# Kernel optimization log

Measured on AMD Instinct MI355X. Metric: run time of the kernel, lower is better.

Reference implementation:

```python
import jax, jax.numpy as jnp
import numpy as np

NUM_HEADS = 8
D_CONV = 4
NORMALIZER = 16.0
LN_EPS = 1e-5


def setup_inputs() -> dict:
    key = jax.random.key(0)
    ks = jax.random.split(key, 9)
    B, L, E = 4, 2048, 1024
    dk = E // 2
    return {
        "x": jax.random.normal(ks[0], (B, L, E), jnp.float32),
        "conv_w": jax.random.normal(ks[1], (E, D_CONV), jnp.float32) * 0.3,
        "wq": jax.random.normal(ks[2], (E, dk), jnp.float32) * 0.02,
        "wkg": jax.random.normal(ks[3], (E, dk), jnp.float32) * 0.02,
        "wv": jax.random.normal(ks[4], (E, E), jnp.float32) * 0.02,
        "wg": jax.random.normal(ks[5], (E, E), jnp.float32) * 0.02,
        "bg": jax.random.normal(ks[6], (E,), jnp.float32) * 0.02,
        "wout": jax.random.normal(ks[7], (E, E), jnp.float32) * 0.02,
        "aug_balance": jax.random.normal(ks[8], (dk,), jnp.float32) * 0.1,
    }


def _causal_dwconv_silu(x, w):
    # x: [B, L, E]; w: [E, W] depthwise kernel. Causal: left-pad W-1 zeros.
    xt = jnp.transpose(x, (0, 2, 1))  # [B, E, L]
    y = jax.lax.conv_general_dilated(
        xt, w[:, None, :], window_strides=(1,), padding=[(w.shape[1] - 1, 0)],
        feature_group_count=x.shape[-1], dimension_numbers=("NCH", "OIH", "NCH"))
    return jnp.transpose(jax.nn.silu(y), (0, 2, 1))  # [B, L, E]


def _gla(q, k, v, gk, scale):
    # Gated linear attention recurrence (fused_chunk_gla math):
    #   S_t = S_{t-1} * exp(gk_t)[:, None] + k_t (outer) v_t
    #   o_t = (scale * q_t) @ S_t
    # q, k, gk: [B,H,L,Dk]; v: [B,H,L,Dv]
    B, H, L, Dk = q.shape
    Dv = v.shape[-1]

    def step(S, inp):
        qt, kt, vt, gt = inp  # [B,H,Dk], [B,H,Dk], [B,H,Dv], [B,H,Dk]
        S = S * jnp.exp(gt)[..., None] + kt[..., None] * vt[..., None, :]
        ot = jnp.einsum("bhk,bhkv->bhv", qt * scale, S)
        return S, ot

    mv = lambda a: jnp.moveaxis(a, 2, 0)  # L to leading axis for scan
    S0 = jnp.zeros((B, H, Dk, Dv), q.dtype)
    _, o = jax.lax.scan(step, S0, (mv(q), mv(k), mv(v), mv(gk)))
    return jnp.moveaxis(o, 0, 2)  # [B,H,L,Dv]


def reference(x, conv_w, wq, wkg, wv, wg, bg, wout, aug_balance):
    B, L, E = x.shape
    H = NUM_HEADS
    xc = _causal_dwconv_silu(x, conv_w)
    q = xc @ wq            # [B,L,dk]
    kg = xc @ wkg          # [B,L,dk]
    v = xc @ wv            # [B,L,E]
    g = xc @ wg + bg       # [B,L,E]

    gk = jax.nn.log_sigmoid(kg) / NORMALIZER
    k = 1.0 - jnp.exp(gk)

    dkh = q.shape[-1] // H  # key_dim per head
    to_heads = lambda t: t.reshape(B, L, H, -1).transpose(0, 2, 1, 3)
    qh, kh, vh, gkh = to_heads(q), to_heads(k), to_heads(v), to_heads(gk)

    scale = dkh ** -0.5
    o = _gla(qh, kh, vh, gkh, scale)  # [B,H,L,head_dim]

    # Augmented term: aug_w[b,h,l] = sum_d q[b,h,l,d] * aug[h,d] * k[b,h,l,d]
    aug = aug_balance.reshape(H, dkh)
    aug_w = jnp.einsum("bhld,hd,bhld->bhl", qh, aug, kh)
    o = o + jax.nn.sigmoid(aug_w[..., None] * vh)

    # LayerNorm over head_dim, no affine
    mu = o.mean(-1, keepdims=True)
    var = o.var(-1, keepdims=True)
    o = (o - mu) * jax.lax.rsqrt(var + LN_EPS)

    o = o.transpose(0, 2, 1, 3).reshape(B, L, E)
    return (jax.nn.silu(g) * o) @ wout
```

## Files before the change

kernel.cpp:

```cpp
#include <hip/hip_runtime.h>
#include <stdint.h>

typedef unsigned short u16;
typedef unsigned int u32;
typedef __attribute__((ext_vector_type(4))) float f32x4;
typedef __attribute__((ext_vector_type(8))) short short8;
typedef __attribute__((ext_vector_type(8))) _Float16 f16x8;

#define H 8
#define LSEQ 2048
#define E 1024
#define DK 512
#define DVH 128
#define DKH 64
#define NCHUNK 32
#define MROWS 8192
#define LN_EPS 1e-5f

static __device__ __forceinline__ float bf2f(u16 u) {
    union { float f; u32 i; } v; v.i = ((u32)u) << 16; return v.f;
}
static __device__ __forceinline__ u16 f2bf(float f) {
    union { float f; u32 i; } v; v.f = f;
    u32 r = v.i + 0x7FFFu + ((v.i >> 16) & 1u);
    return (u16)(r >> 16);
}

__global__ __launch_bounds__(256) void k_conv(const float* __restrict__ x,
                                              const float* __restrict__ cw,
                                              u16* __restrict__ xc) {
    const int l0 = blockIdx.x * 64;
    const int c  = blockIdx.y * 256 + threadIdx.x;
    const int b  = blockIdx.z;
    const f32x4 w = *(const f32x4*)(cw + c * 4);
    const float* base = x + (size_t)b * LSEQ * E + c;
    u16* ob = xc + (size_t)b * LSEQ * E + c;
    float x3 = (l0 >= 3) ? base[(size_t)(l0 - 3) * E] : 0.f;
    float x2 = (l0 >= 2) ? base[(size_t)(l0 - 2) * E] : 0.f;
    float x1 = (l0 >= 1) ? base[(size_t)(l0 - 1) * E] : 0.f;
#pragma unroll 8
    for (int r = 0; r < 64; r++) {
        const float x0 = base[(size_t)(l0 + r) * E];
        float a = x3 * w[0];
        a = fmaf(x2, w[1], a);
        a = fmaf(x1, w[2], a);
        a = fmaf(x0, w[3], a);
        const float s = a / (1.f + __expf(-a));
        ob[(size_t)(l0 + r) * E] = f2bf(s);
        x3 = x2; x2 = x1; x1 = x0;
    }
}

__global__ __launch_bounds__(256) void k_transpose_all(const float* __restrict__ wq,
                                                       const float* __restrict__ wkg,
                                                       const float* __restrict__ wv,
                                                       const float* __restrict__ wg,
                                                       const float* __restrict__ wout,
                                                       u16* __restrict__ wcat,
                                                       u16* __restrict__ woutT) {
    __shared__ float tile[32][33];
    const int z = blockIdx.z;
    const float* src; u16* dst; int Ncols;
    if (z == 0)      { src = wq;   dst = wcat;                        Ncols = 512; }
    else if (z == 1) { src = wkg;  dst = wcat + (size_t)512 * 1024;   Ncols = 512; }
    else if (z == 2) { src = wv;   dst = wcat + (size_t)1024 * 1024;  Ncols = 1024; }
    else if (z == 3) { src = wg;   dst = wcat + (size_t)2048 * 1024;  Ncols = 1024; }
    else             { src = wout; dst = woutT;                       Ncols = 1024; }
    const int n0 = blockIdx.x * 32, k0 = blockIdx.y * 32;
    if (n0 >= Ncols) return;
    const int K = 1024;
    const int tx = threadIdx.x & 31, ty = threadIdx.x >> 5;
#pragma unroll
    for (int p = 0; p < 4; p++) {
        const int r = p * 8 + ty;
        tile[r][tx] = src[(size_t)(k0 + r) * Ncols + n0 + tx];
    }
    __syncthreads();
#pragma unroll
    for (int p = 0; p < 4; p++) {
        const int rn = p * 8 + ty;
        dst[(size_t)(n0 + rn) * K + k0 + tx] = f2bf(tile[tx][rn]);
    }
}

__global__ __launch_bounds__(512, 1) void k_gemm0(const u16* __restrict__ A,
                                                  const u16* __restrict__ Bt,
                                                  u16* __restrict__ oQ, u16* __restrict__ oKG,
                                                  u16* __restrict__ oV, u16* __restrict__ oSG,
                                                  const float* __restrict__ bg) {
    const int K = 1024;
    __shared__ __align__(16) u16 smem[4][16384];
    const int tid = threadIdx.x;
    const int lane = tid & 63, wv = tid >> 6;
    const int wm = wv >> 2, wn = wv & 3;

    const int id = blockIdx.x;
    const int local = id >> 3;
    const int bx = ((id & 7) << 3) | (local & 7);
    const int by = local >> 3;

    const size_t rowBase = (size_t)bx * 128;
    const size_t colBase = (size_t)by * 384;

    const int rowIn = lane >> 2;
    const int uIn = lane & 3;

    auto stageA = [&](int hh) {
        u16* slotA = &smem[hh & 3][0];
        const u16* g = A + rowBase * K + hh * 32;
        const int row = wv * 16 + rowIn;
        const int sg = uIn ^ ((row >> 1) & 3);
        __builtin_amdgcn_global_load_lds(
            (const __attribute__((address_space(1))) void*)(g + (size_t)row * K + sg * 8),
            (__attribute__((address_space(3))) void*)(slotA + wv * 512), 16, 0, 0);
    };
    auto stageB = [&](int hh) {
        u16* slotB = &smem[hh & 3][4096];
        const u16* g = Bt + colBase * K + hh * 32;
#pragma unroll
        for (int i = 0; i < 3; i++) {
            const int row = i * 128 + wv * 16 + rowIn;
            const int sg = uIn ^ ((row >> 1) & 3);
            __builtin_amdgcn_global_load_lds(
                (const __attribute__((address_space(1))) void*)(g + (size_t)row * K + sg * 8),
                (__attribute__((address_space(3))) void*)(slotB + i * 4096 + wv * 512), 16, 0, 0);
        }
    };

    f32x4 acc[4][6];
#pragma unroll
    for (int m = 0; m < 4; m++)
#pragma unroll
        for (int n = 0; n < 6; n++) acc[m][n] = (f32x4){0.f, 0.f, 0.f, 0.f};

    const int rsub = lane & 15;
    const int cgl = lane >> 4;

    stageA(0); stageB(0);
    stageA(1); stageB(1);
    stageA(2); stageB(2);

    const int NT2 = K >> 5;
    for (int h = 0; h < NT2; h++) {
        const int rem = NT2 - 1 - h;
        if (rem >= 2)      asm volatile("s_waitcnt vmcnt(8)" ::: "memory");
        else if (rem == 1) asm volatile("s_waitcnt vmcnt(4)" ::: "memory");
        else               asm volatile("s_waitcnt vmcnt(0)" ::: "memory");
        asm volatile("s_barrier" ::: "memory");
        const u16* As = &smem[h & 3][0];
        const u16* Bs = As + 4096;
        short8 af[4], bfr[6];
#pragma unroll
        for (int mi = 0; mi < 4; mi++) {
            const int row = wm * 64 + mi * 16 + rsub;
            const int g = cgl ^ ((row >> 1) & 3);
            af[mi] = *(const short8*)(As + row * 32 + g * 8);
        }
#pragma unroll
        for (int ni = 0; ni < 6; ni++) {
            const int row = wn * 96 + ni * 16 + rsub;
            const int g = cgl ^ ((row >> 1) & 3);
            bfr[ni] = *(const short8*)(Bs + row * 32 + g * 8);
        }
        if (h + 3 < NT2) { stageA(h + 3); stageB(h + 3); }
        __builtin_amdgcn_s_setprio(1);
#pragma unroll
        for (int mi = 0; mi < 4; mi++)
#pragma unroll
            for (int ni = 0; ni < 6; ni++)
                acc[mi][ni] = __builtin_amdgcn_mfma_f32_16x16x32_bf16(af[mi], bfr[ni], acc[mi][ni], 0, 0, 0);
        __builtin_amdgcn_s_setprio(0);
    }

    const int r0 = (lane >> 4) * 4;
    u16* lds = &smem[0][0];
    __syncthreads();
#pragma unroll
    for (int ni = 0; ni < 6; ni++) {
        const int colg = (int)colBase + wn * 96 + ni * 16 + rsub;
        const bool isSG = (colg >= 2048);
        const float bgv = isSG ? bg[colg - 2048] : 0.f;
#pragma unroll
        for (int mi = 0; mi < 4; mi++) {
            const int lcol = wn * 96 + ni * 16 + rsub;
#pragma unroll
            for (int r = 0; r < 4; r++) {
                const int lrow = wm * 64 + mi * 16 + r0 + r;
                float val = acc[mi][ni][r];
                if (isSG) { const float y = val + bgv; val = y / (1.f + __expf(-y)); }
                lds[lrow * 384 + lcol] = f2bf(val);
            }
        }
    }
    __syncthreads();
    if (lane < 48) {
        const int col = (int)colBase + lane * 8;
        u16* seg; int stride; int c0;
        if (col < 512)       { seg = oQ;  stride = 512;  c0 = col; }
        else if (col < 1024) { seg = oKG; stride = 512;  c0 = col - 512; }
        else if (col < 2048) { seg = oV;  stride = 1024; c0 = col - 1024; }
        else                 { seg = oSG; stride = 1024; c0 = col - 2048; }
#pragma unroll
        for (int rr = 0; rr < 16; rr++) {
            const int lrow = wv * 16 + rr;
            const uint4 vv = *(const uint4*)(lds + lrow * 384 + lane * 8);
            *(uint4*)(seg + (rowBase + lrow) * (size_t)stride + c0) = vv;
        }
    }
}

__global__ __launch_bounds__(512, 1) void k_gemm1(const u16* __restrict__ A,
                                                  const u16* __restrict__ Bt,
                                                  float* __restrict__ oF) {
    const int K = 1024, N = 1024;
    __shared__ __align__(16) u16 smem[4][12288];
    const int tid = threadIdx.x;
    const int lane = tid & 63, wv = tid >> 6;
    const int wm = wv >> 1, wn = wv & 1;

    const int id = blockIdx.y * gridDim.x + blockIdx.x;
    const int bx = ((id & 7) << 2) | ((id >> 3) & 3);
    const int by = id >> 5;

    const size_t rowBase = (size_t)bx * 256;
    const size_t colBase = (size_t)by * 128;

    auto stageA = [&](int hh) {
        u16* slotA = &smem[hh & 3][0];
        const u16* g = A + rowBase * K + hh * 32;
#pragma unroll
        for (int i = 0; i < 2; i++) {
            const int r = i * 128 + wv * 16 + (lane >> 2);
            const int sg = (lane & 3) ^ ((r >> 1) & 3);
            __builtin_amdgcn_global_load_lds(
                (const __attribute__((address_space(1))) void*)(g + (size_t)r * K + sg * 8),
                (__attribute__((address_space(3))) void*)(slotA + i * 4096 + wv * 512), 16, 0, 0);
        }
    };
    auto stageB = [&](int hh) {
        u16* slotB = &smem[hh & 3][8192];
        const u16* g = Bt + colBase * K + hh * 32;
        const int r = wv * 16 + (lane >> 2);
        const int sg = (lane & 3) ^ ((r >> 1) & 3);
        __builtin_amdgcn_global_load_lds(
            (const __attribute__((address_space(1))) void*)(g + (size_t)r * K + sg * 8),
            (__attribute__((address_space(3))) void*)(slotB + wv * 512), 16, 0, 0);
    };

    f32x4 acc[4][4];
#pragma unroll
    for (int m = 0; m < 4; m++)
#pragma unroll
        for (int n = 0; n < 4; n++) acc[m][n] = (f32x4){0.f, 0.f, 0.f, 0.f};

    const int rsub = lane & 15;
    const int cgl = lane >> 4;

    stageA(0); stageB(0);
    stageA(1); stageB(1);
    stageA(2); stageB(2);

    const int NT2 = K >> 5;
    for (int h = 0; h < NT2; h++) {
        const int rem = NT2 - 1 - h;
        if (rem >= 2)      asm volatile("s_waitcnt vmcnt(6)" ::: "memory");
        else if (rem == 1) asm volatile("s_waitcnt vmcnt(3)" ::: "memory");
        else               asm volatile("s_waitcnt vmcnt(0)" ::: "memory");
        asm volatile("s_barrier" ::: "memory");
        const u16* As = &smem[h & 3][0];
        const u16* Bs = As + 8192;
        short8 af[4], bfr[4];
#pragma unroll
        for (int mi = 0; mi < 4; mi++) {
            const int row = wm * 64 + mi * 16 + rsub;
            const int g = cgl ^ ((row >> 1) & 3);
            af[mi] = *(const short8*)(As + row * 32 + g * 8);
        }
#pragma unroll
        for (int ni = 0; ni < 4; ni++) {
            const int row = wn * 64 + ni * 16 + rsub;
            const int g = cgl ^ ((row >> 1) & 3);
            bfr[ni] = *(const short8*)(Bs + row * 32 + g * 8);
        }
        if (h + 3 < NT2) { stageA(h + 3); stageB(h + 3); }
        __builtin_amdgcn_s_setprio(1);
#pragma unroll
        for (int mi = 0; mi < 4; mi++)
#pragma unroll
            for (int ni = 0; ni < 4; ni++)
                acc[mi][ni] = __builtin_amdgcn_mfma_f32_16x16x32_bf16(af[mi], bfr[ni], acc[mi][ni], 0, 0, 0);
        __builtin_amdgcn_s_setprio(0);
    }

    const int r0 = (lane >> 4) * 4;
#pragma unroll
    for (int mi = 0; mi < 4; mi++)
#pragma unroll
        for (int ni = 0; ni < 4; ni++) {
            const size_t col = colBase + wn * 64 + ni * 16 + rsub;
#pragma unroll
            for (int r = 0; r < 4; r++) {
                const size_t row = rowBase + wm * 64 + mi * 16 + r0 + r;
                oF[row * (size_t)N + col] = acc[mi][ni][r];
            }
        }
}

__global__ __launch_bounds__(256) void k_gla1(const u16* __restrict__ q,
                                              const u16* __restrict__ kg,
                                              const u16* __restrict__ v,
                                              const float* __restrict__ aug,
                                              u16* __restrict__ qt,
                                              u16* __restrict__ obuf,
                                              float* __restrict__ Sd,
                                              float* __restrict__ Dc,
                                              float* __restrict__ augw) {
    __shared__ __align__(16) float    s_f[64][68];
    __shared__ __align__(16) _Float16 s_q[64][72];
    __shared__ __align__(16) _Float16 s_k[64][72];
    __shared__ __align__(16) _Float16 s_kT[64][72];
    __shared__ __align__(16) _Float16 s_a[64][72];
    __shared__ __align__(16) _Float16 s_vT[128][72];
    const int c = blockIdx.x, bh = blockIdx.y;
    const int b = bh >> 3, h = bh & 7;
    const int tid = threadIdx.x;
    const size_t rowBase = (size_t)b * LSEQ + c * 64;
    const size_t sdBase = (size_t)bh * NCHUNK + c;

    const int tA = tid >> 2, g4 = tid & 3;
    uint4 qr0, qr1;
    {
        const int d0 = g4 * 16;
        const u16* kp = kg + (rowBase + tA) * DK + h * 64 + d0;
        const uint4 k0 = *(const uint4*)kp;
        const uint4 k1 = *(const uint4*)(kp + 8);
        const u16 kv[16] = {
            (u16)(k0.x & 0xffff), (u16)(k0.x >> 16), (u16)(k0.y & 0xffff), (u16)(k0.y >> 16),
            (u16)(k0.z & 0xffff), (u16)(k0.z >> 16), (u16)(k0.w & 0xffff), (u16)(k0.w >> 16),
            (u16)(k1.x & 0xffff), (u16)(k1.x >> 16), (u16)(k1.y & 0xffff), (u16)(k1.y >> 16),
            (u16)(k1.z & 0xffff), (u16)(k1.z >> 16), (u16)(k1.w & 0xffff), (u16)(k1.w >> 16) };
#pragma unroll
        for (int j = 0; j < 16; j++) {
            const float xk = bf2f(kv[j]);
            const float ls = fminf(xk, 0.f) - __logf(1.f + __expf(-fabsf(xk)));
            s_f[tA][d0 + j] = ls * (1.f / 16.f);
        }
        const u16* qp = q + (rowBase + tA) * DK + h * 64 + d0;
        qr0 = *(const uint4*)qp;
        qr1 = *(const uint4*)(qp + 8);

        const int dv0 = g4 * 32;
        const u16* vp = v + (rowBase + tA) * E + h * 128 + dv0;
#pragma unroll
        for (int j8 = 0; j8 < 32; j8 += 8) {
            const uint4 u = *(const uint4*)(vp + j8);
            s_vT[dv0 + j8 + 0][tA] = (_Float16)bf2f((u16)(u.x & 0xffff));
            s_vT[dv0 + j8 + 1][tA] = (_Float16)bf2f((u16)(u.x >> 16));
            s_vT[dv0 + j8 + 2][tA] = (_Float16)bf2f((u16)(u.y & 0xffff));
            s_vT[dv0 + j8 + 3][tA] = (_Float16)bf2f((u16)(u.y >> 16));
            s_vT[dv0 + j8 + 4][tA] = (_Float16)bf2f((u16)(u.z & 0xffff));
            s_vT[dv0 + j8 + 5][tA] = (_Float16)bf2f((u16)(u.z >> 16));
            s_vT[dv0 + j8 + 6][tA] = (_Float16)bf2f((u16)(u.w & 0xffff));
            s_vT[dv0 + j8 + 7][tA] = (_Float16)bf2f((u16)(u.w >> 16));
        }
    }
    __syncthreads();

    {
        const int d = tid >> 2, qseg = tid & 3;
        float part = 0.f;
#pragma unroll
        for (int j = 0; j < 16; j++) part += s_f[qseg * 16 + j][d];
        float incl = part;
        const float u1 = __shfl_up(incl, 1, 4); if (qseg >= 1) incl += u1;
        const float u2 = __shfl_up(incl, 2, 4); if (qseg >= 2) incl += u2;
        float run = incl - part;
#pragma unroll
        for (int j = 0; j < 16; j++) {
            const int t = qseg * 16 + j;
            const float g = s_f[t][d];
            run += g;
            const float kk = 1.f - __expf(g);
            const float ktil = kk * __expf(-run);
            s_k[t][d] = (_Float16)ktil;
            s_kT[d][t] = (_Float16)ktil;
            s_a[t][d] = (_Float16)kk;
            s_f[t][d] = run;
        }
    }
    __syncthreads();

    {
        const int t = tA, d0 = g4 * 16;
        const u16 qv16[16] = {
            (u16)(qr0.x & 0xffff), (u16)(qr0.x >> 16), (u16)(qr0.y & 0xffff), (u16)(qr0.y >> 16),
            (u16)(qr0.z & 0xffff), (u16)(qr0.z >> 16), (u16)(qr0.w & 0xffff), (u16)(qr0.w >> 16),
            (u16)(qr1.x & 0xffff), (u16)(qr1.x >> 16), (u16)(qr1.y & 0xffff), (u16)(qr1.y >> 16),
            (u16)(qr1.z & 0xffff), (u16)(qr1.z >> 16), (u16)(qr1.w & 0xffff), (u16)(qr1.w >> 16) };
        float qv[16];
        float augp = 0.f;
#pragma unroll
        for (int j = 0; j < 16; j++) {
            const int d = d0 + j;
            const float qraw = bf2f(qv16[j]);
            const float L = s_f[t][d];
            const float kk = (float)s_a[t][d];
            const float qtv = qraw * __expf(L) * 0.125f;
            s_q[t][d] = (_Float16)qtv;
            qv[j] = qtv;
            augp = fmaf(qraw * aug[h * 64 + d], kk, augp);
        }
        u16* qto = qt + (rowBase + t) * DK + h * 64 + d0;
#pragma unroll
        for (int j8 = 0; j8 < 16; j8 += 8) {
            uint4 u;
            u.x = (u32)f2bf(qv[j8 + 0]) | ((u32)f2bf(qv[j8 + 1]) << 16);
            u.y = (u32)f2bf(qv[j8 + 2]) | ((u32)f2bf(qv[j8 + 3]) << 16);
            u.z = (u32)f2bf(qv[j8 + 4]) | ((u32)f2bf(qv[j8 + 5]) << 16);
            u.w = (u32)f2bf(qv[j8 + 6]) | ((u32)f2bf(qv[j8 + 7]) << 16);
            *(uint4*)(qto + j8) = u;
        }
        augp += __shfl_xor(augp, 1);
        augp += __shfl_xor(augp, 2);
        if ((tid & 3) == 0) augw[(size_t)bh * LSEQ + c * 64 + t] = augp;
    }
    __syncthreads();

    const int wv = tid >> 6, lane = tid & 63;
    const int rsub = lane & 15, kq8 = (lane >> 4) * 8, r0 = (lane >> 4) * 4;
    {
#pragma unroll
        for (int si = 0; si < 4; si++) {
            if (si <= wv) {
                f32x4 acc = (f32x4){0.f, 0.f, 0.f, 0.f};
#pragma unroll
                for (int kk = 0; kk < 2; kk++) {
                    const f16x8 af = *(const f16x8*)&s_q[wv * 16 + rsub][kk * 32 + kq8];
                    const f16x8 bf = *(const f16x8*)&s_k[si * 16 + rsub][kk * 32 + kq8];
                    acc = __builtin_amdgcn_mfma_f32_16x16x32_f16(af, bf, acc, 0, 0, 0);
                }
                const int scol = si * 16 + rsub;
#pragma unroll
                for (int r = 0; r < 4; r++) {
                    const int trow = wv * 16 + r0 + r;
                    const float val = (scol <= trow) ? acc[r] : 0.f;
                    s_a[trow][scol] = (_Float16)val;
                }
            } else {
#pragma unroll
                for (int r = 0; r < 4; r++)
                    s_a[wv * 16 + r0 + r][si * 16 + rsub] = (_Float16)0.f;
            }
        }
    }
    __syncthreads();

    {
        f32x4 oacc[8];
#pragma unroll
        for (int n = 0; n < 8; n++) oacc[n] = (f32x4){0.f, 0.f, 0.f, 0.f};
        const f16x8 a0 = *(const f16x8*)&s_a[wv * 16 + rsub][kq8];
        const f16x8 a1 = *(const f16x8*)&s_a[wv * 16 + rsub][32 + kq8];
#pragma unroll
        for (int n = 0; n < 8; n++) {
            const f16x8 b0 = *(const f16x8*)&s_vT[n * 16 + rsub][kq8];
            const f16x8 b1 = *(const f16x8*)&s_vT[n * 16 + rsub][32 + kq8];
            oacc[n] = __builtin_amdgcn_mfma_f32_16x16x32_f16(a0, b0, oacc[n], 0, 0, 0);
            oacc[n] = __builtin_amdgcn_mfma_f32_16x16x32_f16(a1, b1, oacc[n], 0, 0, 0);
        }
        u16* ob = obuf + ((size_t)bh * LSEQ + c * 64) * DVH;
#pragma unroll
        for (int n = 0; n < 8; n++) {
            const int dv = n * 16 + rsub;
#pragma unroll
            for (int r = 0; r < 4; r++) {
                const int trow = wv * 16 + r0 + r;
                ob[(size_t)trow * DVH + dv] = f2bf(oacc[n][r]);
            }
        }
    }

    {
        f32x4 sacc[8];
#pragma unroll
        for (int n = 0; n < 8; n++) sacc[n] = (f32x4){0.f, 0.f, 0.f, 0.f};
        const f16x8 a0 = *(const f16x8*)&s_kT[wv * 16 + rsub][kq8];
        const f16x8 a1 = *(const f16x8*)&s_kT[wv * 16 + rsub][32 + kq8];
#pragma unroll
        for (int n = 0; n < 8; n++) {
            const f16x8 b0 = *(const f16x8*)&s_vT[n * 16 + rsub][kq8];
            const f16x8 b1 = *(const f16x8*)&s_vT[n * 16 + rsub][32 + kq8];
            sacc[n] = __builtin_amdgcn_mfma_f32_16x16x32_f16(a0, b0, sacc[n], 0, 0, 0);
            sacc[n] = __builtin_amdgcn_mfma_f32_16x16x32_f16(a1, b1, sacc[n], 0, 0, 0);
        }
        float dend[4];
#pragma unroll
        for (int r = 0; r < 4; r++) dend[r] = __expf(s_f[63][wv * 16 + r0 + r]);
#pragma unroll
        for (int n = 0; n < 8; n++) {
            const int dv = n * 16 + rsub;
#pragma unroll
            for (int r = 0; r < 4; r++) {
                const int d = wv * 16 + r0 + r;
                Sd[(sdBase * DKH + d) * DVH + dv] = sacc[n][r] * dend[r];
            }
        }
        if (rsub == 0) {
#pragma unroll
            for (int r = 0; r < 4; r++) {
                const int d = wv * 16 + r0 + r;
                Dc[sdBase * DKH + d] = dend[r];
            }
        }
    }
}

__global__ __launch_bounds__(256) void k_gla2(const float* __restrict__ Sd,
                                              u16* __restrict__ Ss,
                                              const float* __restrict__ Dc) {
    const int cid = blockIdx.x * 256 + threadIdx.x;
    const int bh = cid >> 13;
    const int e = cid & 8191;
    const int d = e >> 7;
    float run = 0.f;
    const size_t base = (size_t)bh * NCHUNK * 8192 + e;
    for (int c = 0; c < NCHUNK; c++) {
        const size_t idx = base + (size_t)c * 8192;
        const float dl = Sd[idx];
        Ss[idx] = f2bf(run);
        run = fmaf(Dc[((size_t)bh * NCHUNK + c) * DKH + d], run, dl);
    }
}

__global__ __launch_bounds__(256) void k_gla3(const u16* __restrict__ qt,
                                              const u16* __restrict__ v,
                                              const u16* __restrict__ sg,
                                              const u16* __restrict__ obuf,
                                              const u16* __restrict__ Ss,
                                              const float* __restrict__ augw,
                                              u16* __restrict__ a2) {
    __shared__ __align__(16) _Float16 s_ST[128][72];
    __shared__ __align__(16) _Float16 s_qr[64][72];
    __shared__ __align__(16) float    s_O2[64][132];
    const int c = blockIdx.x, bh = blockIdx.y;
    const int b = bh >> 3, h = bh & 7;
    const int tid = threadIdx.x;
    const size_t rowBase = (size_t)b * LSEQ + c * 64;
    {
        const int d = tid >> 2, dv0 = (tid & 3) * 32;
        const u16* sp = Ss + (((size_t)bh * NCHUNK + c) * DKH + d) * DVH + dv0;
#pragma unroll
        for (int j8 = 0; j8 < 32; j8 += 8) {
            const uint4 u = *(const uint4*)(sp + j8);
            s_ST[dv0 + j8 + 0][d] = (_Float16)bf2f((u16)(u.x & 0xffff));
            s_ST[dv0 + j8 + 1][d] = (_Float16)bf2f((u16)(u.x >> 16));
            s_ST[dv0 + j8 + 2][d] = (_Float16)bf2f((u16)(u.y & 0xffff));
            s_ST[dv0 + j8 + 3][d] = (_Float16)bf2f((u16)(u.y >> 16));
            s_ST[dv0 + j8 + 4][d] = (_Float16)bf2f((u16)(u.z & 0xffff));
            s_ST[dv0 + j8 + 5][d] = (_Float16)bf2f((u16)(u.z >> 16));
            s_ST[dv0 + j8 + 6][d] = (_Float16)bf2f((u16)(u.w & 0xffff));
            s_ST[dv0 + j8 + 7][d] = (_Float16)bf2f((u16)(u.w >> 16));
        }
    }
    {
        const int t = tid >> 2, d0 = (tid & 3) * 16;
        const u16* qp = qt + (rowBase + t) * DK + h * 64 + d0;
        const uint4 q0 = *(const uint4*)qp;
        const uint4 q1 = *(const uint4*)(qp + 8);
        const u16 qv[16] = {
            (u16)(q0.x & 0xffff), (u16)(q0.x >> 16), (u16)(q0.y & 0xffff), (u16)(q0.y >> 16),
            (u16)(q0.z & 0xffff), (u16)(q0.z >> 16), (u16)(q0.w & 0xffff), (u16)(q0.w >> 16),
            (u16)(q1.x & 0xffff), (u16)(q1.x >> 16), (u16)(q1.y & 0xffff), (u16)(q1.y >> 16),
            (u16)(q1.z & 0xffff), (u16)(q1.z >> 16), (u16)(q1.w & 0xffff), (u16)(q1.w >> 16) };
#pragma unroll
        for (int j = 0; j < 16; j++) s_qr[t][d0 + j] = (_Float16)bf2f(qv[j]);
    }
    __syncthreads();
    {
        const int wv = tid >> 6, lane = tid & 63;
        const int rsub = lane & 15, kq8 = (lane >> 4) * 8, r0 = (lane >> 4) * 4;
        const f16x8 a0 = *(const f16x8*)&s_qr[wv * 16 + rsub][kq8];
        const f16x8 a1 = *(const f16x8*)&s_qr[wv * 16 + rsub][32 + kq8];
#pragma unroll
        for (int n = 0; n < 8; n++) {
            f32x4 acc = (f32x4){0.f, 0.f, 0.f, 0.f};
            const f16x8 b0 = *(const f16x8*)&s_ST[n * 16 + rsub][kq8];
            const f16x8 b1 = *(const f16x8*)&s_ST[n * 16 + rsub][32 + kq8];
            acc = __builtin_amdgcn_mfma_f32_16x16x32_f16(a0, b0, acc, 0, 0, 0);
            acc = __builtin_amdgcn_mfma_f32_16x16x32_f16(a1, b1, acc, 0, 0, 0);
            const int dv = n * 16 + rsub;
#pragma unroll
            for (int r = 0; r < 4; r++) s_O2[wv * 16 + r0 + r][dv] = acc[r];
        }
    }
    __syncthreads();
    const int t = tid >> 2, dv0 = (tid & 3) * 32;
    float o[32];
    const u16* op = obuf + ((size_t)bh * LSEQ + c * 64 + t) * DVH + dv0;
#pragma unroll
    for (int j8 = 0; j8 < 32; j8 += 8) {
        const uint4 u = *(const uint4*)(op + j8);
        o[j8 + 0] = bf2f((u16)(u.x & 0xffff)); o[j8 + 1] = bf2f((u16)(u.x >> 16));
        o[j8 + 2] = bf2f((u16)(u.y & 0xffff)); o[j8 + 3] = bf2f((u16)(u.y >> 16));
        o[j8 + 4] = bf2f((u16)(u.z & 0xffff)); o[j8 + 5] = bf2f((u16)(u.z >> 16));
        o[j8 + 6] = bf2f((u16)(u.w & 0xffff)); o[j8 + 7] = bf2f((u16)(u.w >> 16));
    }
#pragma unroll
    for (int j = 0; j < 32; j += 4) {
        const f32x4 sv = *(const f32x4*)&s_O2[t][dv0 + j];
        o[j + 0] += sv[0]; o[j + 1] += sv[1]; o[j + 2] += sv[2]; o[j + 3] += sv[3];
    }
    const float aw = augw[(size_t)bh * LSEQ + c * 64 + t];
    const u16* vp = v + (rowBase + t) * E + h * 128 + dv0;
#pragma unroll
    for (int j8 = 0; j8 < 32; j8 += 8) {
        const uint4 u = *(const uint4*)(vp + j8);
        const float vv[8] = {
            bf2f((u16)(u.x & 0xffff)), bf2f((u16)(u.x >> 16)),
            bf2f((u16)(u.y & 0xffff)), bf2f((u16)(u.y >> 16)),
            bf2f((u16)(u.z & 0xffff)), bf2f((u16)(u.z >> 16)),
            bf2f((u16)(u.w & 0xffff)), bf2f((u16)(u.w >> 16)) };
#pragma unroll
        for (int j = 0; j < 8; j++)
            o[j8 + j] += 1.f / (1.f + __expf(-aw * vv[j]));
    }
    float sum = 0.f;
#pragma unroll
    for (int j = 0; j < 32; j++) sum += o[j];
    sum += __shfl_xor(sum, 1); sum += __shfl_xor(sum, 2);
    const float mu = sum * (1.f / 128.f);
    float sq = 0.f;
#pragma unroll
    for (int j = 0; j < 32; j++) { const float dlt = o[j] - mu; sq = fmaf(dlt, dlt, sq); }
    sq += __shfl_xor(sq, 1); sq += __shfl_xor(sq, 2);
    const float rs = rsqrtf(sq * (1.f / 128.f) + LN_EPS);
    const u16* sp2 = sg + (rowBase + t) * E + h * 128 + dv0;
    u16* ap = a2 + (rowBase + t) * E + h * 128 + dv0;
#pragma unroll
    for (int j8 = 0; j8 < 32; j8 += 8) {
        const uint4 us = *(const uint4*)(sp2 + j8);
        const float sv[8] = {
            bf2f((u16)(us.x & 0xffff)), bf2f((u16)(us.x >> 16)),
            bf2f((u16)(us.y & 0xffff)), bf2f((u16)(us.y >> 16)),
            bf2f((u16)(us.z & 0xffff)), bf2f((u16)(us.z >> 16)),
            bf2f((u16)(us.w & 0xffff)), bf2f((u16)(us.w >> 16)) };
        uint4 u;
        u.x = (u32)f2bf(sv[0] * ((o[j8 + 0] - mu) * rs)) | ((u32)f2bf(sv[1] * ((o[j8 + 1] - mu) * rs)) << 16);
        u.y = (u32)f2bf(sv[2] * ((o[j8 + 2] - mu) * rs)) | ((u32)f2bf(sv[3] * ((o[j8 + 3] - mu) * rs)) << 16);
        u.z = (u32)f2bf(sv[4] * ((o[j8 + 4] - mu) * rs)) | ((u32)f2bf(sv[5] * ((o[j8 + 5] - mu) * rs)) << 16);
        u.w = (u32)f2bf(sv[6] * ((o[j8 + 6] - mu) * rs)) | ((u32)f2bf(sv[7] * ((o[j8 + 7] - mu) * rs)) << 16);
        *(uint4*)(ap + j8) = u;
    }
}

extern "C" void kernel_launch(void* const* d_in, const int* in_sizes, int n_in,
                              void* d_out, int out_size, void* d_ws, size_t ws_size,
                              hipStream_t stream) {
    const float* x      = (const float*)d_in[0];
    const float* conv_w = (const float*)d_in[1];
    const float* wq     = (const float*)d_in[2];
    const float* wkg    = (const float*)d_in[3];
    const float* wv     = (const float*)d_in[4];
    const float* wg     = (const float*)d_in[5];
    const float* bg     = (const float*)d_in[6];
    const float* wout   = (const float*)d_in[7];
    const float* aug    = (const float*)d_in[8];

    char* ws = (char*)d_ws;
    size_t off = 0;
    auto alloc = [&](size_t bytes) -> char* {
        char* p = ws + off;
        off += (bytes + 255) & ~(size_t)255;
        return p;
    };
    u16* xc    = (u16*)alloc((size_t)MROWS * E * 2);
    u16* wcat  = (u16*)alloc((size_t)3072 * E * 2);
    u16* woutT = (u16*)alloc((size_t)E * E * 2);
    u16* qb    = (u16*)alloc((size_t)MROWS * DK * 2);
    u16* kgb   = (u16*)alloc((size_t)MROWS * DK * 2);
    u16* vb    = (u16*)alloc((size_t)MROWS * E * 2);
    u16* sgb   = (u16*)alloc((size_t)MROWS * E * 2);
    u16* qtb   = (u16*)alloc((size_t)MROWS * DK * 2);
    u16* obuf  = (u16*)alloc((size_t)32 * LSEQ * DVH * 2);
    u16* Ssb   = (u16*)alloc((size_t)32 * NCHUNK * DKH * DVH * 2);
    float* Dc  = (float*)alloc((size_t)32 * NCHUNK * DKH * 4);
    float* augw= (float*)alloc((size_t)32 * LSEQ * 4);
    u16* a2    = qb;
    float* Sd  = (float*)d_out;

    k_conv<<<dim3(LSEQ / 64, E / 256, 4), 256, 0, stream>>>(x, conv_w, xc);
    k_transpose_all<<<dim3(32, 32, 5), 256, 0, stream>>>(wq, wkg, wv, wg, wout, wcat, woutT);
    k_gemm0<<<512, 512, 0, stream>>>(xc, wcat, qb, kgb, vb, sgb, bg);
    k_gla1<<<dim3(NCHUNK, 32), 256, 0, stream>>>(qb, kgb, vb, aug, qtb, obuf, Sd, Dc, augw);
    k_gla2<<<1024, 256, 0, stream>>>(Sd, Ssb, Dc);
    k_gla3<<<dim3(NCHUNK, 32), 256, 0, stream>>>(qtb, vb, sgb, obuf, Ssb, augw, a2);
    k_gemm1<<<dim3(32, 8), 512, 0, stream>>>(a2, woutT, (float*)d_out);
}
```

Before: 161.3 us.

## Enlarge gemm0 block tile to 256x384 with three-stage LDS pipeline

The fused QKV/gate projection GEMM now uses 256-row tiles instead of 128, halving the grid to 256 blocks so each block reuses its B tile across twice as many rows. The LDS ring drops from four stages to three to fit the larger tiles, with a reworked waitcnt schedule. The A fragments are now loaded inside the MFMA loop. The epilogue is split into two barrier-separated halves through LDS with coalesced 128-column stores. The trade-off is fewer blocks than CUs on MI355X (256 CUs, so about one wave of blocks) and higher register pressure from the 8x6 accumulator array.

Result: slower. 167.4 us (+3.8%).

```diff
diff --git a/kernel.cpp b/kernel.cpp
--- a/kernel.cpp
+++ b/kernel.cpp
@@ -89,122 +89,128 @@
                                                   u16* __restrict__ oV, u16* __restrict__ oSG,
                                                   const float* __restrict__ bg) {
     const int K = 1024;
-    __shared__ __align__(16) u16 smem[4][16384];
+    __shared__ __align__(16) u16 smem[3][20480];
     const int tid = threadIdx.x;
     const int lane = tid & 63, wv = tid >> 6;
     const int wm = wv >> 2, wn = wv & 3;
 
     const int id = blockIdx.x;
     const int local = id >> 3;
-    const int bx = ((id & 7) << 3) | (local & 7);
-    const int by = local >> 3;
-
-    const size_t rowBase = (size_t)bx * 128;
+    const int bx = ((id & 7) << 2) | (local & 3);
+    const int by = local >> 2;
+
+    const size_t rowBase = (size_t)bx * 256;
     const size_t colBase = (size_t)by * 384;
 
-    const int rowIn = lane >> 2;
-    const int uIn = lane & 3;
-
-    auto stageA = [&](int hh) {
-        u16* slotA = &smem[hh & 3][0];
-        const u16* g = A + rowBase * K + hh * 32;
-        const int row = wv * 16 + rowIn;
-        const int sg = uIn ^ ((row >> 1) & 3);
-        __builtin_amdgcn_global_load_lds(
-            (const __attribute__((address_space(1))) void*)(g + (size_t)row * K + sg * 8),
-            (__attribute__((address_space(3))) void*)(slotA + wv * 512), 16, 0, 0);
+    auto stage = [&](int hh, int sl) {
+        u16* slotA = &smem[sl][0];
+        u16* slotB = &smem[sl][8192];
+        const u16* gA = A + rowBase * K + hh * 32;
+        const u16* gB = Bt + colBase * K + hh * 32;
+#pragma unroll
+        for (int i = 0; i < 2; i++) {
+            const int u = i * 512 + wv * 64 + lane;
+            const int row = u >> 2;
+            const int sg = (lane & 3) ^ ((row >> 1) & 3);
+            __builtin_amdgcn_global_load_lds(
+                (const __attribute__((address_space(1))) void*)(gA + (size_t)row * K + sg * 8),
+                (__attribute__((address_space(3))) void*)(slotA + (i * 512 + wv * 64) * 8), 16, 0, 0);
+        }
+#pragma unroll
+        for (int i = 0; i < 3; i++) {
+            const int u = i * 512 + wv * 64 + lane;
+            const int row = u >> 2;
+            const int sg = (lane & 3) ^ ((row >> 1) & 3);
+            __builtin_amdgcn_global_load_lds(
+                (const __attribute__((address_space(1))) void*)(gB + (size_t)row * K + sg * 8),
+                (__attribute__((address_space(3))) void*)(slotB + (i * 512 + wv * 64) * 8), 16, 0, 0);
+        }
     };
-    auto stageB = [&](int hh) {
-        u16* slotB = &smem[hh & 3][4096];
-        const u16* g = Bt + colBase * K + hh * 32;
-#pragma unroll
-        for (int i = 0; i < 3; i++) {
-            const int row = i * 128 + wv * 16 + rowIn;
-            const int sg = uIn ^ ((row >> 1) & 3);
-            __builtin_amdgcn_global_load_lds(
-                (const __attribute__((address_space(1))) void*)(g + (size_t)row * K + sg * 8),
-                (__attribute__((address_space(3))) void*)(slotB + i * 4096 + wv * 512), 16, 0, 0);
-        }
-    };
-
-    f32x4 acc[4][6];
-#pragma unroll
-    for (int m = 0; m < 4; m++)
+
+    f32x4 acc[8][6];
+#pragma unroll
+    for (int m = 0; m < 8; m++)
 #pragma unroll
         for (int n = 0; n < 6; n++) acc[m][n] = (f32x4){0.f, 0.f, 0.f, 0.f};
 
     const int rsub = lane & 15;
     const int cgl = lane >> 4;
 
-    stageA(0); stageB(0);
-    stageA(1); stageB(1);
-    stageA(2); stageB(2);
+    stage(0, 0); stage(1, 1);
 
     const int NT2 = K >> 5;
+    int sl = 0;
     for (int h = 0; h < NT2; h++) {
-        const int rem = NT2 - 1 - h;
-        if (rem >= 2)      asm volatile("s_waitcnt vmcnt(8)" ::: "memory");
-        else if (rem == 1) asm volatile("s_waitcnt vmcnt(4)" ::: "memory");
-        else               asm volatile("s_waitcnt vmcnt(0)" ::: "memory");
+        if (h + 1 < NT2) asm volatile("s_waitcnt vmcnt(5)" ::: "memory");
+        else             asm volatile("s_waitcnt vmcnt(0)" ::: "memory");
         asm volatile("s_barrier" ::: "memory");
-        const u16* As = &smem[h & 3][0];
-        const u16* Bs = As + 4096;
-        short8 af[4], bfr[6];
-#pragma unroll
-        for (int mi = 0; mi < 4; mi++) {
-            const int row = wm * 64 + mi * 16 + rsub;
-            const int g = cgl ^ ((row >> 1) & 3);
-            af[mi] = *(const short8*)(As + row * 32 + g * 8);
-        }
+        const u16* As = &smem[sl][0];
+        const u16* Bs = &smem[sl][8192];
+        short8 bfr[6];
 #pragma unroll
         for (int ni = 0; ni < 6; ni++) {
             const int row = wn * 96 + ni * 16 + rsub;
             const int g = cgl ^ ((row >> 1) & 3);
             bfr[ni] = *(const short8*)(Bs + row * 32 + g * 8);
         }
-        if (h + 3 < NT2) { stageA(h + 3); stageB(h + 3); }
+        if (h + 2 < NT2) {
+            const int sl2 = (sl + 2) % 3;
+            stage(h + 2, sl2);
+        }
         __builtin_amdgcn_s_setprio(1);
 #pragma unroll
-        for (int mi = 0; mi < 4; mi++)
+        for (int mi = 0; mi < 8; mi++) {
+            const int row = wm * 128 + mi * 16 + rsub;
+            const int g = cgl ^ ((row >> 1) & 3);
+            const short8 af = *(const short8*)(As + row * 32 + g * 8);
 #pragma unroll
             for (int ni = 0; ni < 6; ni++)
-                acc[mi][ni] = __builtin_amdgcn_mfma_f32_16x16x32_bf16(af[mi], bfr[ni], acc[mi][ni], 0, 0, 0);
+                acc[mi][ni] = __builtin_amdgcn_mfma_f32_16x16x32_bf16(af, bfr[ni], acc[mi][ni], 0, 0, 0);
+        }
         __builtin_amdgcn_s_setprio(0);
+        sl = (sl + 1) % 3;
     }
 
     const int r0 = (lane >> 4) * 4;
     u16* lds = &smem[0][0];
-    __syncthreads();
-#pragma unroll
-    for (int ni = 0; ni < 6; ni++) {
-        const int colg = (int)colBase + wn * 96 + ni * 16 + rsub;
-        const bool isSG = (colg >= 2048);
-        const float bgv = isSG ? bg[colg - 2048] : 0.f;
-#pragma unroll
-        for (int mi = 0; mi < 4; mi++) {
-            const int lcol = wn * 96 + ni * 16 + rsub;
-#pragma unroll
-            for (int r = 0; r < 4; r++) {
-                const int lrow = wm * 64 + mi * 16 + r0 + r;
-                float val = acc[mi][ni][r];
-                if (isSG) { const float y = val + bgv; val = y / (1.f + __expf(-y)); }
-                lds[lrow * 384 + lcol] = f2bf(val);
+#pragma unroll
+    for (int p = 0; p < 2; p++) {
+        asm volatile("s_barrier" ::: "memory");
+        if (wm == p) {
+#pragma unroll
+            for (int ni = 0; ni < 6; ni++) {
+                const int colg = (int)colBase + wn * 96 + ni * 16 + rsub;
+                const bool isSG = (colg >= 2048);
+                const float bgv = isSG ? bg[colg - 2048] : 0.f;
+                const int lcol = wn * 96 + ni * 16 + rsub;
+#pragma unroll
+                for (int mi = 0; mi < 8; mi++) {
+#pragma unroll
+                    for (int r = 0; r < 4; r++) {
+                        const int lrow = mi * 16 + r0 + r;
+                        float val = acc[mi][ni][r];
+                        if (isSG) { const float y = val + bgv; val = y / (1.f + __expf(-y)); }
+                        lds[lrow * 384 + lcol] = f2bf(val);
+                    }
+                }
             }
         }
-    }
-    __syncthreads();
-    if (lane < 48) {
-        const int col = (int)colBase + lane * 8;
-        u16* seg; int stride; int c0;
-        if (col < 512)       { seg = oQ;  stride = 512;  c0 = col; }
-        else if (col < 1024) { seg = oKG; stride = 512;  c0 = col - 512; }
-        else if (col < 2048) { seg = oV;  stride = 1024; c0 = col - 1024; }
-        else                 { seg = oSG; stride = 1024; c0 = col - 2048; }
-#pragma unroll
-        for (int rr = 0; rr < 16; rr++) {
-            const int lrow = wv * 16 + rr;
-            const uint4 vv = *(const uint4*)(lds + lrow * 384 + lane * 8);
-            *(uint4*)(seg + (rowBase + lrow) * (size_t)stride + c0) = vv;
+        asm volatile("s_barrier" ::: "memory");
+#pragma unroll
+        for (int pp = 0; pp < 3; pp++) {
+            const int cbase = (int)colBase + pp * 128;
+            u16* seg; int stride; int c0;
+            if (cbase < 512)       { seg = oQ;  stride = 512;  c0 = cbase; }
+            else if (cbase < 1024) { seg = oKG; stride = 512;  c0 = cbase - 512; }
+            else if (cbase < 2048) { seg = oV;  stride = 1024; c0 = cbase - 1024; }
+            else                   { seg = oSG; stride = 1024; c0 = cbase - 2048; }
+#pragma unroll
+            for (int i = 0; i < 4; i++) {
+                const int unit = i * 512 + tid;
+                const int row = unit >> 4, u = unit & 15;
+                const uint4 vv = *(const uint4*)(lds + row * 384 + pp * 128 + u * 8);
+                *(uint4*)(seg + (rowBase + p * 128 + row) * (size_t)stride + c0 + u * 8) = vv;
+            }
         }
     }
 }
@@ -690,7 +696,7 @@
 
     k_conv<<<dim3(LSEQ / 64, E / 256, 4), 256, 0, stream>>>(x, conv_w, xc);
     k_transpose_all<<<dim3(32, 32, 5), 256, 0, stream>>>(wq, wkg, wv, wg, wout, wcat, woutT);
-    k_gemm0<<<512, 512, 0, stream>>>(xc, wcat, qb, kgb, vb, sgb, bg);
+    k_gemm0<<<256, 512, 0, stream>>>(xc, wcat, qb, kgb, vb, sgb, bg);
     k_gla1<<<dim3(NCHUNK, 32), 256, 0, stream>>>(qb, kgb, vb, aug, qtb, obuf, Sd, Dc, augw);
     k_gla2<<<1024, 256, 0, stream>>>(Sd, Ssb, Dc);
     k_gla3<<<dim3(NCHUNK, 32), 256, 0, stream>>>(qtb, vb, sgb, obuf, Ssb, augw, a2);
```

## Shrink gemm0 to double-buffered LDS and split epilogue into two column passes

Applied to the files above, without the earlier changes.

The fused QKV/gate GEMM drops from a 4-slot LDS ring with three tiles in flight to a 2-slot double buffer with one tile prefetched, and waits for vmcnt(0) every iteration. The epilogue now stages half the 384-column tile at a time through a 192-wide LDS buffer. The output store is rewritten so all 512 threads write coalesced 16-byte chunks instead of 48 lanes per wave. This cuts LDS from 128KB to 64KB, which may allow more occupancy or lower pressure, but it weakens latency hiding in the main loop.

Result: slower. 171.5 us (+6.3%).

```diff
diff --git a/kernel.cpp b/kernel.cpp
--- a/kernel.cpp
+++ b/kernel.cpp
@@ -16,6 +16,9 @@
 #define NCHUNK 32
 #define MROWS 8192
 #define LN_EPS 1e-5f
+
+#define AS1 __attribute__((address_space(1)))
+#define AS3 __attribute__((address_space(3)))
 
 static __device__ __forceinline__ float bf2f(u16 u) {
     union { float f; u32 i; } v; v.i = ((u32)u) << 16; return v.f;
@@ -89,7 +92,7 @@
                                                   u16* __restrict__ oV, u16* __restrict__ oSG,
                                                   const float* __restrict__ bg) {
     const int K = 1024;
-    __shared__ __align__(16) u16 smem[4][16384];
+    __shared__ __align__(16) u16 smem[2][16384];
     const int tid = threadIdx.x;
     const int lane = tid & 63, wv = tid >> 6;
     const int wm = wv >> 2, wn = wv & 3;
@@ -105,25 +108,25 @@
     const int rowIn = lane >> 2;
     const int uIn = lane & 3;
 
-    auto stageA = [&](int hh) {
-        u16* slotA = &smem[hh & 3][0];
-        const u16* g = A + rowBase * K + hh * 32;
-        const int row = wv * 16 + rowIn;
-        const int sg = uIn ^ ((row >> 1) & 3);
-        __builtin_amdgcn_global_load_lds(
-            (const __attribute__((address_space(1))) void*)(g + (size_t)row * K + sg * 8),
-            (__attribute__((address_space(3))) void*)(slotA + wv * 512), 16, 0, 0);
-    };
-    auto stageB = [&](int hh) {
-        u16* slotB = &smem[hh & 3][4096];
-        const u16* g = Bt + colBase * K + hh * 32;
+    auto stage = [&](int hh) {
+        u16* slotA = &smem[hh & 1][0];
+        u16* slotB = &smem[hh & 1][4096];
+        const u16* gA = A + rowBase * K + hh * 32;
+        const u16* gB = Bt + colBase * K + hh * 32;
+        {
+            const int row = wv * 16 + rowIn;
+            const int sg = uIn ^ ((row >> 1) & 3);
+            __builtin_amdgcn_global_load_lds(
+                (const AS1 void*)(gA + (size_t)row * K + sg * 8),
+                (AS3 void*)(slotA + wv * 512), 16, 0, 0);
+        }
 #pragma unroll
         for (int i = 0; i < 3; i++) {
             const int row = i * 128 + wv * 16 + rowIn;
             const int sg = uIn ^ ((row >> 1) & 3);
             __builtin_amdgcn_global_load_lds(
-                (const __attribute__((address_space(1))) void*)(g + (size_t)row * K + sg * 8),
-                (__attribute__((address_space(3))) void*)(slotB + i * 4096 + wv * 512), 16, 0, 0);
+                (const AS1 void*)(gB + (size_t)row * K + sg * 8),
+                (AS3 void*)(slotB + i * 4096 + wv * 512), 16, 0, 0);
         }
     };
 
@@ -136,18 +139,13 @@
     const int rsub = lane & 15;
     const int cgl = lane >> 4;
 
-    stageA(0); stageB(0);
-    stageA(1); stageB(1);
-    stageA(2); stageB(2);
+    stage(0);
 
     const int NT2 = K >> 5;
     for (int h = 0; h < NT2; h++) {
-        const int rem = NT2 - 1 - h;
-        if (rem >= 2)      asm volatile("s_waitcnt vmcnt(8)" ::: "memory");
-        else if (rem == 1) asm volatile("s_waitcnt vmcnt(4)" ::: "memory");
-        else               asm volatile("s_waitcnt vmcnt(0)" ::: "memory");
+        asm volatile("s_waitcnt vmcnt(0)" ::: "memory");
         asm volatile("s_barrier" ::: "memory");
-        const u16* As = &smem[h & 3][0];
+        const u16* As = &smem[h & 1][0];
         const u16* Bs = As + 4096;
         short8 af[4], bfr[6];
 #pragma unroll
@@ -162,7 +160,7 @@
             const int g = cgl ^ ((row >> 1) & 3);
             bfr[ni] = *(const short8*)(Bs + row * 32 + g * 8);
         }
-        if (h + 3 < NT2) { stageA(h + 3); stageB(h + 3); }
+        if (h + 1 < NT2) stage(h + 1);
         __builtin_amdgcn_s_setprio(1);
 #pragma unroll
         for (int mi = 0; mi < 4; mi++)
@@ -174,37 +172,45 @@
 
     const int r0 = (lane >> 4) * 4;
     u16* lds = &smem[0][0];
-    __syncthreads();
-#pragma unroll
-    for (int ni = 0; ni < 6; ni++) {
-        const int colg = (int)colBase + wn * 96 + ni * 16 + rsub;
-        const bool isSG = (colg >= 2048);
-        const float bgv = isSG ? bg[colg - 2048] : 0.f;
-#pragma unroll
-        for (int mi = 0; mi < 4; mi++) {
-            const int lcol = wn * 96 + ni * 16 + rsub;
-#pragma unroll
-            for (int r = 0; r < 4; r++) {
-                const int lrow = wm * 64 + mi * 16 + r0 + r;
-                float val = acc[mi][ni][r];
-                if (isSG) { const float y = val + bgv; val = y / (1.f + __expf(-y)); }
-                lds[lrow * 384 + lcol] = f2bf(val);
+#pragma unroll
+    for (int cp = 0; cp < 2; cp++) {
+        asm volatile("s_barrier" ::: "memory");
+        if ((wn >> 1) == cp) {
+            const int wnl = wn & 1;
+#pragma unroll
+            for (int ni = 0; ni < 6; ni++) {
+                const int gcol = (int)colBase + wn * 96 + ni * 16 + rsub;
+                const bool isSG = (gcol >= 2048);
+                const float bgv = isSG ? bg[gcol - 2048] : 0.f;
+                const int lcol = wnl * 96 + ni * 16 + rsub;
+#pragma unroll
+                for (int mi = 0; mi < 4; mi++) {
+#pragma unroll
+                    for (int r = 0; r < 4; r++) {
+                        const int lrow = wm * 64 + mi * 16 + r0 + r;
+                        float val = acc[mi][ni][r];
+                        if (isSG) { const float y = val + bgv; val = y / (1.f + __expf(-y)); }
+                        lds[lrow * 192 + lcol] = f2bf(val);
+                    }
+                }
             }
         }
-    }
-    __syncthreads();
-    if (lane < 48) {
-        const int col = (int)colBase + lane * 8;
-        u16* seg; int stride; int c0;
-        if (col < 512)       { seg = oQ;  stride = 512;  c0 = col; }
-        else if (col < 1024) { seg = oKG; stride = 512;  c0 = col - 512; }
-        else if (col < 2048) { seg = oV;  stride = 1024; c0 = col - 1024; }
-        else                 { seg = oSG; stride = 1024; c0 = col - 2048; }
-#pragma unroll
-        for (int rr = 0; rr < 16; rr++) {
-            const int lrow = wv * 16 + rr;
-            const uint4 vv = *(const uint4*)(lds + lrow * 384 + lane * 8);
-            *(uint4*)(seg + (rowBase + lrow) * (size_t)stride + c0) = vv;
+        asm volatile("s_barrier" ::: "memory");
+#pragma unroll
+        for (int sp = 0; sp < 3; sp++) {
+            const int gc = (int)colBase + cp * 192 + sp * 64;
+            u16* seg; int stride; int c0;
+            if (gc < 512)       { seg = oQ;  stride = 512;  c0 = gc; }
+            else if (gc < 1024) { seg = oKG; stride = 512;  c0 = gc - 512; }
+            else if (gc < 2048) { seg = oV;  stride = 1024; c0 = gc - 1024; }
+            else                { seg = oSG; stride = 1024; c0 = gc - 2048; }
+#pragma unroll
+            for (int i = 0; i < 2; i++) {
+                const int u = i * 512 + tid;
+                const int row = u >> 3, uu = u & 7;
+                const uint4 vv = *(const uint4*)(lds + row * 192 + sp * 64 + uu * 8);
+                *(uint4*)(seg + (rowBase + row) * (size_t)stride + c0 + uu * 8) = vv;
+            }
         }
     }
 }
@@ -233,8 +239,8 @@
             const int r = i * 128 + wv * 16 + (lane >> 2);
             const int sg = (lane & 3) ^ ((r >> 1) & 3);
             __builtin_amdgcn_global_load_lds(
-                (const __attribute__((address_space(1))) void*)(g + (size_t)r * K + sg * 8),
-                (__attribute__((address_space(3))) void*)(slotA + i * 4096 + wv * 512), 16, 0, 0);
+                (const AS1 void*)(g + (size_t)r * K + sg * 8),
+                (AS3 void*)(slotA + i * 4096 + wv * 512), 16, 0, 0);
         }
     };
     auto stageB = [&](int hh) {
@@ -243,8 +249,8 @@
         const int r = wv * 16 + (lane >> 2);
         const int sg = (lane & 3) ^ ((r >> 1) & 3);
         __builtin_amdgcn_global_load_lds(
-            (const __attribute__((address_space(1))) void*)(g + (size_t)r * K + sg * 8),
-            (__attribute__((address_space(3))) void*)(slotB + wv * 512), 16, 0, 0);
+            (const AS1 void*)(g + (size_t)r * K + sg * 8),
+            (AS3 void*)(slotB + wv * 512), 16, 0, 0);
     };
 
     f32x4 acc[4][4];
```
